# Performance work log

Measured on AMD Instinct MI355X. Metric: run time of the kernel, lower is better.

The kernel has to match this reference:

```python
import jax, jax.numpy as jnp
import numpy as np

IN_C = 128
OUT_C = 128
MEM = 512
HID = MEM // 2  # 256, per ParameterGenerator hidden_channels = memory_size // 2
T = 8          # number of edge types (keys of edge_feas_dict)
N = 500_000


def setup_inputs() -> dict:
    key = jax.random.key(0)
    ks = jax.random.split(key, 16)
    s = 0.02
    inp = {
        "x": jax.random.normal(ks[0], (N, IN_C), dtype=jnp.float32),
        "type_vec": jax.random.randint(ks[1], (N,), 0, T),
        "edge_feas": jax.random.normal(ks[2], (T, MEM), dtype=jnp.float32),
        # weight_generator MLP: Linear(MEM,HID) -> ReLU -> Linear(HID,HID) -> ReLU -> Linear(HID, IN_C*OUT_C)
        "wg_w1": jax.random.normal(ks[3], (MEM, HID), dtype=jnp.float32) * s,
        "wg_b1": jnp.zeros((HID,), dtype=jnp.float32),
        "wg_w2": jax.random.normal(ks[4], (HID, HID), dtype=jnp.float32) * s,
        "wg_b2": jnp.zeros((HID,), dtype=jnp.float32),
        "wg_w3": jax.random.normal(ks[5], (HID, IN_C * OUT_C), dtype=jnp.float32) * s,
        "wg_b3": jnp.zeros((IN_C * OUT_C,), dtype=jnp.float32),
        # bias_generator MLP: Linear(MEM,HID) -> ReLU -> Linear(HID,HID) -> ReLU -> Linear(HID, OUT_C)
        "bg_w1": jax.random.normal(ks[6], (MEM, HID), dtype=jnp.float32) * s,
        "bg_b1": jnp.zeros((HID,), dtype=jnp.float32),
        "bg_w2": jax.random.normal(ks[7], (HID, HID), dtype=jnp.float32) * s,
        "bg_b2": jnp.zeros((HID,), dtype=jnp.float32),
        "bg_w3": jax.random.normal(ks[8], (HID, OUT_C), dtype=jnp.float32) * s,
        "bg_b3": jnp.zeros((OUT_C,), dtype=jnp.float32),
    }
    return inp


def _mlp(m, w1, b1, w2, b2, w3, b3):
    h = jax.nn.relu(m @ w1 + b1)
    h = jax.nn.relu(h @ w2 + b2)
    return h @ w3 + b3


def reference(x, type_vec, edge_feas,
              wg_w1, wg_b1, wg_w2, wg_b2, wg_w3, wg_b3,
              bg_w1, bg_b1, bg_w2, bg_b2, bg_w3, bg_b3):
    # Generate per-type weights [T, IN_C, OUT_C] and biases [T, OUT_C]
    W = _mlp(edge_feas, wg_w1, wg_b1, wg_w2, wg_b2, wg_w3, wg_b3).reshape(T, IN_C, OUT_C)
    B = _mlp(edge_feas, bg_w1, bg_b1, bg_w2, bg_b2, bg_w3, bg_b3)  # [T, OUT_C]
    # Masked per-type linear, scattered back: out[n] = x[n] @ W[type_vec[n]] + B[type_vec[n]]
    out = jnp.zeros((x.shape[0], OUT_C), dtype=x.dtype)
    for t in range(T):  # small fixed set of types
        yt = x @ W[t] + B[t]
        out = jnp.where((type_vec == t)[:, None], yt, out)
    return out
```

## Files before the change

### kernel.cpp

```cpp
#include <hip/hip_runtime.h>
#include <hip/hip_bf16.h>

#define NT 8
#define MEMC 512
#define HID 256
#define C 128

typedef __attribute__((ext_vector_type(8))) short short8;
typedef __attribute__((ext_vector_type(4))) float f32x4;

__device__ inline short f2bf(float f) {
    __hip_bfloat16 h = __float2bfloat16(f);
    union { __hip_bfloat16 b; short s; } u;
    u.b = h;
    return u.s;
}

__global__ __launch_bounds__(256) void k1_init_genh(
    const float* __restrict__ edge_feas,
    const float* __restrict__ wg_w1, const float* __restrict__ wg_b1,
    const float* __restrict__ wg_w2, const float* __restrict__ wg_b2,
    const float* __restrict__ bg_w1, const float* __restrict__ bg_b1,
    const float* __restrict__ bg_w2, const float* __restrict__ bg_b2,
    int* __restrict__ hist, int* __restrict__ idx, int idx_cap,
    float* __restrict__ h_wg, float* __restrict__ h_bg,
    int n_init_blocks)
{
    int b = blockIdx.x, tid = threadIdx.x;
    if (b < n_init_blocks) {
        int pos = b * 1024 + tid * 4;
        if (pos < idx_cap) {
            int4 v = make_int4(-1, -1, -1, -1);
            *(int4*)(idx + pos) = v;
        }
        return;
    }
    if (b == n_init_blocks) {
        if (tid < NT) hist[tid] = 0;
        return;
    }
    int gb = b - n_init_blocks - 1;
    int t = gb & 7;
    int gen = gb >> 3;
    const float* w1 = gen ? bg_w1 : wg_w1;
    const float* b1 = gen ? bg_b1 : wg_b1;
    const float* w2 = gen ? bg_w2 : wg_w2;
    const float* b2 = gen ? bg_b2 : wg_b2;
    float* hout = gen ? h_bg : h_wg;

    __shared__ float m[MEMC];
    __shared__ float h1[HID];
    m[tid]       = edge_feas[t * MEMC + tid];
    m[tid + 256] = edge_feas[t * MEMC + tid + 256];
    __syncthreads();

    float a0 = b1[tid], a1 = 0.f;
    #pragma unroll 4
    for (int k = 0; k < MEMC; k += 2) {
        a0 += m[k]     * w1[k * HID + tid];
        a1 += m[k + 1] * w1[(k + 1) * HID + tid];
    }
    h1[tid] = fmaxf(a0 + a1, 0.f);
    __syncthreads();

    a0 = b2[tid]; a1 = 0.f;
    #pragma unroll 4
    for (int k = 0; k < HID; k += 2) {
        a0 += h1[k]     * w2[k * HID + tid];
        a1 += h1[k + 1] * w2[(k + 1) * HID + tid];
    }
    hout[t * HID + tid] = fmaxf(a0 + a1, 0.f);
}

__global__ __launch_bounds__(256) void k2_hist_genw(
    const int* __restrict__ type_vec, int N,
    const float* __restrict__ h_wg, const float* __restrict__ h_bg,
    const float* __restrict__ wg_w3, const float* __restrict__ wg_b3,
    const float* __restrict__ bg_w3, const float* __restrict__ bg_b3,
    int* __restrict__ hist, short* __restrict__ Wkn, float* __restrict__ Bias,
    int n_hist_blocks)
{
    int b = blockIdx.x, tid = threadIdx.x;
    if (b < n_hist_blocks) {
        __shared__ int lh[NT];
        if (tid < NT) lh[tid] = 0;
        __syncthreads();
        int base = b * 1024 + tid;
        #pragma unroll
        for (int i = 0; i < 4; ++i) {
            int n = base + i * 256;
            if (n < N) atomicAdd(&lh[type_vec[n]], 1);
        }
        __syncthreads();
        if (tid < NT) atomicAdd(&hist[tid], lh[tid]);
        return;
    }
    int gb = b - n_hist_blocks;
    if (gb < 128) {
        int chunk = gb >> 1;
        int t0 = (gb & 1) * 4;
        __shared__ float h[4][HID];
        for (int i = tid; i < 4 * HID; i += 256)
            h[i >> 8][i & 255] = h_wg[(t0 + (i >> 8)) * HID + (i & 255)];
        __syncthreads();
        int col = chunk * 256 + tid;
        float a0 = 0.f, a1 = 0.f, a2 = 0.f, a3 = 0.f;
        #pragma unroll 2
        for (int j = 0; j < HID; ++j) {
            float v = wg_w3[j * (C * C) + col];
            a0 += h[0][j] * v;
            a1 += h[1][j] * v;
            a2 += h[2][j] * v;
            a3 += h[3][j] * v;
        }
        float b3 = wg_b3[col];
        Wkn[(t0 + 0) * (C * C) + col] = f2bf(a0 + b3);
        Wkn[(t0 + 1) * (C * C) + col] = f2bf(a1 + b3);
        Wkn[(t0 + 2) * (C * C) + col] = f2bf(a2 + b3);
        Wkn[(t0 + 3) * (C * C) + col] = f2bf(a3 + b3);
        return;
    }
    if (tid < C) {
        for (int t = 0; t < NT; ++t) {
            float acc = bg_b3[tid];
            for (int j = 0; j < HID; ++j)
                acc += h_bg[t * HID + j] * bg_w3[j * C + tid];
            Bias[t * C + tid] = acc;
        }
    }
}

__global__ void k3_scan(const int* __restrict__ hist, int* __restrict__ seg,
                        int* __restrict__ cursor)
{
    if (threadIdx.x == 0) {
        int s = 0;
        for (int t = 0; t < NT; ++t) {
            seg[t] = s;
            s += ((hist[t] + 63) >> 6) << 6;
        }
        seg[NT] = s;
    }
    if (threadIdx.x < NT) cursor[threadIdx.x * 16] = 0;
}

__global__ __launch_bounds__(256) void k4_scatter_transpose(
    const int* __restrict__ type_vec, int N,
    const int* __restrict__ seg, int* __restrict__ cursor,
    int* __restrict__ idx,
    const short* __restrict__ Wkn, short* __restrict__ Wt,
    int n_scatter_blocks)
{
    int b = blockIdx.x, tid = threadIdx.x;
    if (b >= n_scatter_blocks) {
        int t = b - n_scatter_blocks;
        __shared__ short tile[C][C + 8];
        const short* src = Wkn + t * (C * C);
        for (int i = tid; i < C * C; i += 256)
            tile[i >> 7][i & 127] = src[i];
        __syncthreads();
        short* dst = Wt + t * (C * C);
        for (int i = tid; i < C * C; i += 256)
            dst[i] = tile[i & 127][i >> 7];
        return;
    }
    int lane = tid & 63;
    int wave = b * 4 + (tid >> 6);
    int start = wave * 1024;
    if (start >= N) return;

    int cnt[NT];
    #pragma unroll
    for (int t = 0; t < NT; ++t) cnt[t] = 0;
    for (int c = 0; c < 16; ++c) {
        int n = start + c * 64 + lane;
        int mt = (n < N) ? type_vec[n] : NT;
        #pragma unroll
        for (int t = 0; t < NT; ++t)
            cnt[t] += __popcll(__ballot(mt == t));
    }
    int base = 0;
    if (lane < NT) base = atomicAdd(&cursor[lane * 16], cnt[lane]);
    int run[NT];
    #pragma unroll
    for (int t = 0; t < NT; ++t) run[t] = seg[t] + __shfl(base, t, 64);
    unsigned long long below = (1ULL << lane) - 1ULL;
    for (int c = 0; c < 16; ++c) {
        int n = start + c * 64 + lane;
        int mt = (n < N) ? type_vec[n] : NT;
        int mypos = 0;
        #pragma unroll
        for (int t = 0; t < NT; ++t) {
            unsigned long long msk = __ballot(mt == t);
            if (mt == t) mypos = run[t] + __popcll(msk & below);
            run[t] += __popcll(msk);
        }
        if (n < N) idx[mypos] = n;
    }
}

__global__ __launch_bounds__(256) void k5_gemm(
    const float* __restrict__ x, const int* __restrict__ idx,
    const short* __restrict__ Wt, const float* __restrict__ Bias,
    const int* __restrict__ seg, float* __restrict__ out)
{
    int tid = threadIdx.x;
    int lane = tid & 63;
    int w = tid >> 6;
    int block_base = blockIdx.x * 64;
    int total = seg[NT];
    if (block_base >= total) return;

    int t = 0;
    #pragma unroll
    for (int i = 1; i < NT; ++i)
        if (block_base >= seg[i]) t = i;

    int quad = lane >> 4;
    int m16 = lane & 15;
    const short* Wtt = Wt + t * (C * C);

    int arow = idx[block_base + 16 * w + m16];
    bool avalid = arow >= 0;
    const float* xrow = x + (size_t)(avalid ? arow : 0) * C;

    f32x4 acc[8];
    #pragma unroll
    for (int i = 0; i < 8; ++i) acc[i] = (f32x4){0.f, 0.f, 0.f, 0.f};

    #pragma unroll
    for (int kk = 0; kk < 4; ++kk) {
        int k0 = kk * 32 + quad * 8;
        short8 afrag;
        if (avalid) {
            float4 a0 = *(const float4*)(xrow + k0);
            float4 a1 = *(const float4*)(xrow + k0 + 4);
            afrag[0] = f2bf(a0.x); afrag[1] = f2bf(a0.y);
            afrag[2] = f2bf(a0.z); afrag[3] = f2bf(a0.w);
            afrag[4] = f2bf(a1.x); afrag[5] = f2bf(a1.y);
            afrag[6] = f2bf(a1.z); afrag[7] = f2bf(a1.w);
        } else {
            afrag = (short8){0, 0, 0, 0, 0, 0, 0, 0};
        }
        #pragma unroll
        for (int ni = 0; ni < 8; ++ni) {
            short8 bfrag = *(const short8*)(Wtt + (ni * 16 + m16) * C + k0);
            acc[ni] = __builtin_amdgcn_mfma_f32_16x16x32_bf16(afrag, bfrag, acc[ni], 0, 0, 0);
        }
    }

    float bv[8];
    #pragma unroll
    for (int ni = 0; ni < 8; ++ni) bv[ni] = Bias[t * C + ni * 16 + m16];

    int p0 = block_base + 16 * w + quad * 4;
    #pragma unroll
    for (int r = 0; r < 4; ++r) {
        int node = idx[p0 + r];
        if (node < 0) continue;
        float* orow = out + (size_t)node * C;
        #pragma unroll
        for (int ni = 0; ni < 8; ++ni)
            orow[ni * 16 + m16] = acc[ni][r] + bv[ni];
    }
}

extern "C" void kernel_launch(void* const* d_in, const int* in_sizes, int n_in,
                              void* d_out, int out_size, void* d_ws, size_t ws_size,
                              hipStream_t stream)
{
    const float* x         = (const float*)d_in[0];
    const int*   type_vec  = (const int*)d_in[1];
    const float* edge_feas = (const float*)d_in[2];
    const float* wg_w1 = (const float*)d_in[3];
    const float* wg_b1 = (const float*)d_in[4];
    const float* wg_w2 = (const float*)d_in[5];
    const float* wg_b2 = (const float*)d_in[6];
    const float* wg_w3 = (const float*)d_in[7];
    const float* wg_b3 = (const float*)d_in[8];
    const float* bg_w1 = (const float*)d_in[9];
    const float* bg_b1 = (const float*)d_in[10];
    const float* bg_w2 = (const float*)d_in[11];
    const float* bg_b2 = (const float*)d_in[12];
    const float* bg_w3 = (const float*)d_in[13];
    const float* bg_b3 = (const float*)d_in[14];
    float* out = (float*)d_out;
    int N = in_sizes[1];

    char* ws = (char*)d_ws;
    int*   hist   = (int*)(ws + 0);
    int*   seg    = (int*)(ws + 64);
    int*   cursor = (int*)(ws + 128);
    float* h_wg   = (float*)(ws + 1024);
    float* h_bg   = (float*)(ws + 9216);
    float* Bias   = (float*)(ws + 17408);
    short* Wkn    = (short*)(ws + 21504);
    short* Wt     = (short*)(ws + 283648);
    int*   idx    = (int*)(ws + 545792);

    int nblk64  = (N + 63) / 64;
    int idx_cap = (nblk64 + 8) * 64;
    int n_init  = (idx_cap + 1023) / 1024;
    int n_hist  = (N + 1023) / 1024;
    int n_scat  = (n_hist + 3) / 4;

    k1_init_genh<<<n_init + 17, 256, 0, stream>>>(
        edge_feas, wg_w1, wg_b1, wg_w2, wg_b2, bg_w1, bg_b1, bg_w2, bg_b2,
        hist, idx, idx_cap, h_wg, h_bg, n_init);

    k2_hist_genw<<<n_hist + 129, 256, 0, stream>>>(
        type_vec, N, h_wg, h_bg, wg_w3, wg_b3, bg_w3, bg_b3,
        hist, Wkn, Bias, n_hist);

    k3_scan<<<1, 64, 0, stream>>>(hist, seg, cursor);

    k4_scatter_transpose<<<n_scat + 8, 256, 0, stream>>>(
        type_vec, N, seg, cursor, idx, Wkn, Wt, n_scat);

    k5_gemm<<<nblk64 + 8, 256, 0, stream>>>(x, idx, Wt, Bias, seg, out);
}
```

Baseline: 660.1 us.

## Stage gather GEMM through LDS, parallelize weight generator, drop scan kernel

New measurement: 544.9 us. 17.4% less time.

```diff
diff --git a/kernel.cpp b/kernel.cpp
--- a/kernel.cpp
+++ b/kernel.cpp
@@ -7,12 +7,12 @@
 #define C 128
 
 typedef __attribute__((ext_vector_type(8))) short short8;
+typedef __attribute__((ext_vector_type(4))) short short4v;
 typedef __attribute__((ext_vector_type(4))) float f32x4;
 
 __device__ inline short f2bf(float f) {
-    __hip_bfloat16 h = __float2bfloat16(f);
     union { __hip_bfloat16 b; short s; } u;
-    u.b = h;
+    u.b = __float2bfloat16(f);
     return u.s;
 }
 
@@ -22,21 +22,19 @@
     const float* __restrict__ wg_w2, const float* __restrict__ wg_b2,
     const float* __restrict__ bg_w1, const float* __restrict__ bg_b1,
     const float* __restrict__ bg_w2, const float* __restrict__ bg_b2,
-    int* __restrict__ hist, int* __restrict__ idx, int idx_cap,
+    int* __restrict__ hist, int* __restrict__ cursor,
+    int* __restrict__ idx, int idx_cap,
     float* __restrict__ h_wg, float* __restrict__ h_bg,
     int n_init_blocks)
 {
     int b = blockIdx.x, tid = threadIdx.x;
     if (b < n_init_blocks) {
         int pos = b * 1024 + tid * 4;
-        if (pos < idx_cap) {
-            int4 v = make_int4(-1, -1, -1, -1);
-            *(int4*)(idx + pos) = v;
-        }
+        if (pos < idx_cap) *(int4*)(idx + pos) = make_int4(-1, -1, -1, -1);
         return;
     }
     if (b == n_init_blocks) {
-        if (tid < NT) hist[tid] = 0;
+        if (tid < NT) { hist[tid] = 0; cursor[tid * 16] = 0; }
         return;
     }
     int gb = b - n_init_blocks - 1;
@@ -49,27 +47,46 @@
     float* hout = gen ? h_bg : h_wg;
 
     __shared__ float m[MEMC];
+    __shared__ float part[4][HID];
     __shared__ float h1[HID];
     m[tid]       = edge_feas[t * MEMC + tid];
     m[tid + 256] = edge_feas[t * MEMC + tid + 256];
     __syncthreads();
 
-    float a0 = b1[tid], a1 = 0.f;
-    #pragma unroll 4
-    for (int k = 0; k < MEMC; k += 2) {
-        a0 += m[k]     * w1[k * HID + tid];
-        a1 += m[k + 1] * w1[(k + 1) * HID + tid];
-    }
-    h1[tid] = fmaxf(a0 + a1, 0.f);
-    __syncthreads();
-
-    a0 = b2[tid]; a1 = 0.f;
-    #pragma unroll 4
-    for (int k = 0; k < HID; k += 2) {
-        a0 += h1[k]     * w2[k * HID + tid];
-        a1 += h1[k + 1] * w2[(k + 1) * HID + tid];
-    }
-    hout[t * HID + tid] = fmaxf(a0 + a1, 0.f);
+    int w = tid >> 6, l = tid & 63;
+    {
+        float ax = 0.f, ay = 0.f, az = 0.f, aw = 0.f;
+        const float* wp = w1 + (size_t)(w * 128) * HID + 4 * l;
+        #pragma unroll 8
+        for (int k = 0; k < 128; ++k) {
+            float4 v = *(const float4*)(wp + (size_t)k * HID);
+            float mk = m[w * 128 + k];
+            ax += mk * v.x; ay += mk * v.y; az += mk * v.z; aw += mk * v.w;
+        }
+        *(float4*)&part[w][4 * l] = make_float4(ax, ay, az, aw);
+    }
+    __syncthreads();
+    {
+        float s = part[0][tid] + part[1][tid] + part[2][tid] + part[3][tid] + b1[tid];
+        h1[tid] = fmaxf(s, 0.f);
+    }
+    __syncthreads();
+    {
+        float ax = 0.f, ay = 0.f, az = 0.f, aw = 0.f;
+        const float* wp = w2 + (size_t)(w * 64) * HID + 4 * l;
+        #pragma unroll 8
+        for (int k = 0; k < 64; ++k) {
+            float4 v = *(const float4*)(wp + (size_t)k * HID);
+            float hk = h1[w * 64 + k];
+            ax += hk * v.x; ay += hk * v.y; az += hk * v.z; aw += hk * v.w;
+        }
+        *(float4*)&part[w][4 * l] = make_float4(ax, ay, az, aw);
+    }
+    __syncthreads();
+    {
+        float s = part[0][tid] + part[1][tid] + part[2][tid] + part[3][tid] + b2[tid];
+        hout[t * HID + tid] = fmaxf(s, 0.f);
+    }
 }
 
 __global__ __launch_bounds__(256) void k2_hist_genw(
@@ -81,6 +98,8 @@
     int n_hist_blocks)
 {
     int b = blockIdx.x, tid = threadIdx.x;
+    __shared__ float sh[2048];
+    __shared__ float sp[2048];
     if (b < n_hist_blocks) {
         __shared__ int lh[NT];
         if (tid < NT) lh[tid] = 0;
@@ -96,57 +115,62 @@
         return;
     }
     int gb = b - n_hist_blocks;
-    if (gb < 128) {
-        int chunk = gb >> 1;
-        int t0 = (gb & 1) * 4;
-        __shared__ float h[4][HID];
-        for (int i = tid; i < 4 * HID; i += 256)
-            h[i >> 8][i & 255] = h_wg[(t0 + (i >> 8)) * HID + (i & 255)];
-        __syncthreads();
-        int col = chunk * 256 + tid;
-        float a0 = 0.f, a1 = 0.f, a2 = 0.f, a3 = 0.f;
-        #pragma unroll 2
-        for (int j = 0; j < HID; ++j) {
-            float v = wg_w3[j * (C * C) + col];
-            a0 += h[0][j] * v;
-            a1 += h[1][j] * v;
-            a2 += h[2][j] * v;
-            a3 += h[3][j] * v;
-        }
-        float b3 = wg_b3[col];
-        Wkn[(t0 + 0) * (C * C) + col] = f2bf(a0 + b3);
-        Wkn[(t0 + 1) * (C * C) + col] = f2bf(a1 + b3);
-        Wkn[(t0 + 2) * (C * C) + col] = f2bf(a2 + b3);
-        Wkn[(t0 + 3) * (C * C) + col] = f2bf(a3 + b3);
-        return;
-    }
-    if (tid < C) {
-        for (int t = 0; t < NT; ++t) {
-            float acc = bg_b3[tid];
-            for (int j = 0; j < HID; ++j)
-                acc += h_bg[t * HID + j] * bg_w3[j * C + tid];
-            Bias[t * C + tid] = acc;
-        }
-    }
-}
-
-__global__ void k3_scan(const int* __restrict__ hist, int* __restrict__ seg,
-                        int* __restrict__ cursor)
-{
-    if (threadIdx.x == 0) {
-        int s = 0;
-        for (int t = 0; t < NT; ++t) {
-            seg[t] = s;
-            s += ((hist[t] + 63) >> 6) << 6;
-        }
-        seg[NT] = s;
-    }
-    if (threadIdx.x < NT) cursor[threadIdx.x * 16] = 0;
+    if (gb < 256) {
+        for (int i = tid; i < 2048; i += 256) sh[i] = h_wg[i];
+        __syncthreads();
+        int cl = tid & 63, p = tid >> 6;
+        int col = gb * 64 + cl;
+        float acc[NT];
+        #pragma unroll
+        for (int t = 0; t < NT; ++t) acc[t] = 0.f;
+        const float* wp = wg_w3 + (size_t)(p * 64) * (C * C) + col;
+        #pragma unroll 8
+        for (int j = 0; j < 64; ++j) {
+            float v = wp[(size_t)j * (C * C)];
+            #pragma unroll
+            for (int t = 0; t < NT; ++t) acc[t] += sh[t * 256 + p * 64 + j] * v;
+        }
+        #pragma unroll
+        for (int t = 0; t < NT; ++t) sp[p * 512 + t * 64 + cl] = acc[t];
+        __syncthreads();
+        #pragma unroll
+        for (int r = 0; r < 2; ++r) {
+            int o = tid + 256 * r;
+            int t = o >> 6, c2 = o & 63;
+            float s = sp[t * 64 + c2] + sp[512 + t * 64 + c2]
+                    + sp[1024 + t * 64 + c2] + sp[1536 + t * 64 + c2]
+                    + wg_b3[gb * 64 + c2];
+            Wkn[t * (C * C) + gb * 64 + c2] = f2bf(s);
+        }
+        return;
+    }
+    for (int i = tid; i < 2048; i += 256) sh[i] = h_bg[i];
+    __syncthreads();
+    int cl = tid & 127, p = tid >> 7;
+    float acc[NT];
+    #pragma unroll
+    for (int t = 0; t < NT; ++t) acc[t] = 0.f;
+    const float* wp = bg_w3 + (size_t)(p * 128) * C + cl;
+    #pragma unroll 8
+    for (int j = 0; j < 128; ++j) {
+        float v = wp[(size_t)j * C];
+        #pragma unroll
+        for (int t = 0; t < NT; ++t) acc[t] += sh[t * 256 + p * 128 + j] * v;
+    }
+    #pragma unroll
+    for (int t = 0; t < NT; ++t) sp[p * 1024 + t * 128 + cl] = acc[t];
+    __syncthreads();
+    #pragma unroll
+    for (int r = 0; r < 4; ++r) {
+        int o = tid + 256 * r;
+        int t = o >> 7, c2 = o & 127;
+        Bias[t * C + c2] = sp[t * 128 + c2] + sp[1024 + t * 128 + c2] + bg_b3[c2];
+    }
 }
 
 __global__ __launch_bounds__(256) void k4_scatter_transpose(
     const int* __restrict__ type_vec, int N,
-    const int* __restrict__ seg, int* __restrict__ cursor,
+    const int* __restrict__ hist, int* __restrict__ cursor,
     int* __restrict__ idx,
     const short* __restrict__ Wkn, short* __restrict__ Wt,
     int n_scatter_blocks)
@@ -164,6 +188,12 @@
             dst[i] = tile[i & 127][i >> 7];
         return;
     }
+    int seg[NT];
+    {
+        int s = 0;
+        #pragma unroll
+        for (int t = 0; t < NT; ++t) { seg[t] = s; s += ((hist[t] + 63) >> 6) << 6; }
+    }
     int lane = tid & 63;
     int wave = b * 4 + (tid >> 6);
     int start = wave * 1024;
@@ -199,30 +229,73 @@
     }
 }
 
-__global__ __launch_bounds__(256) void k5_gemm(
+#define AS_LD 136
+#define BS_LD 136
+#define CS_LD 132
+
+__global__ __launch_bounds__(256, 3) void k5_gemm(
     const float* __restrict__ x, const int* __restrict__ idx,
     const short* __restrict__ Wt, const float* __restrict__ Bias,
-    const int* __restrict__ seg, float* __restrict__ out)
-{
+    const int* __restrict__ hist, float* __restrict__ out)
+{
+    __shared__ __align__(16) char smem[64 * AS_LD * 2 + 128 * BS_LD * 2];
+    short (*As)[AS_LD] = (short(*)[AS_LD])smem;
+    short (*Bs)[BS_LD] = (short(*)[BS_LD])(smem + 64 * AS_LD * 2);
+    float (*Cs)[CS_LD] = (float(*)[CS_LD])(smem + 64 * AS_LD * 2);
+    __shared__ int ridx[64];
+
     int tid = threadIdx.x;
-    int lane = tid & 63;
-    int w = tid >> 6;
+    int lane = tid & 63, w = tid >> 6;
     int block_base = blockIdx.x * 64;
-    int total = seg[NT];
-    if (block_base >= total) return;
-
+
+    int seg[NT + 1];
+    {
+        int s = 0;
+        #pragma unroll
+        for (int t = 0; t < NT; ++t) { seg[t] = s; s += ((hist[t] + 63) >> 6) << 6; }
+        seg[NT] = s;
+    }
+    if (block_base >= seg[NT]) return;
     int t = 0;
     #pragma unroll
     for (int i = 1; i < NT; ++i)
         if (block_base >= seg[i]) t = i;
 
-    int quad = lane >> 4;
-    int m16 = lane & 15;
-    const short* Wtt = Wt + t * (C * C);
-
-    int arow = idx[block_base + 16 * w + m16];
-    bool avalid = arow >= 0;
-    const float* xrow = x + (size_t)(avalid ? arow : 0) * C;
+    if (tid < 64) ridx[tid] = idx[block_base + tid];
+    __syncthreads();
+
+    {
+        int rbase = 16 * w + (lane >> 5);
+        int c4 = (lane & 31) * 4;
+        #pragma unroll
+        for (int i = 0; i < 8; ++i) {
+            int r = rbase + i * 2;
+            int node = ridx[r];
+            float4 v = make_float4(0.f, 0.f, 0.f, 0.f);
+            if (node >= 0) v = *(const float4*)(x + (size_t)node * C + c4);
+            short4v sv;
+            sv[0] = f2bf(v.x); sv[1] = f2bf(v.y);
+            sv[2] = f2bf(v.z); sv[3] = f2bf(v.w);
+            *(short4v*)&As[r][c4] = sv;
+        }
+    }
+    {
+        int rr = w * 32 + (lane >> 4);
+        int c8 = (lane & 15) * 8;
+        const short* src = Wt + t * (C * C);
+        #pragma unroll
+        for (int i = 0; i < 8; ++i) {
+            int r = rr + i * 4;
+            short8 v = *(const short8*)(src + r * C + c8);
+            *(short8*)&Bs[r][c8] = v;
+        }
+    }
+    __syncthreads();
+
+    int quad = lane >> 4, m16 = lane & 15;
+    float bv[8];
+    #pragma unroll
+    for (int ni = 0; ni < 8; ++ni) bv[ni] = Bias[t * C + ni * 16 + m16];
 
     f32x4 acc[8];
     #pragma unroll
@@ -230,38 +303,36 @@
 
     #pragma unroll
     for (int kk = 0; kk < 4; ++kk) {
-        int k0 = kk * 32 + quad * 8;
-        short8 afrag;
-        if (avalid) {
-            float4 a0 = *(const float4*)(xrow + k0);
-            float4 a1 = *(const float4*)(xrow + k0 + 4);
-            afrag[0] = f2bf(a0.x); afrag[1] = f2bf(a0.y);
-            afrag[2] = f2bf(a0.z); afrag[3] = f2bf(a0.w);
-            afrag[4] = f2bf(a1.x); afrag[5] = f2bf(a1.y);
-            afrag[6] = f2bf(a1.z); afrag[7] = f2bf(a1.w);
-        } else {
-            afrag = (short8){0, 0, 0, 0, 0, 0, 0, 0};
-        }
+        short8 af = *(const short8*)&As[16 * w + m16][kk * 32 + quad * 8];
         #pragma unroll
         for (int ni = 0; ni < 8; ++ni) {
-            short8 bfrag = *(const short8*)(Wtt + (ni * 16 + m16) * C + k0);
-            acc[ni] = __builtin_amdgcn_mfma_f32_16x16x32_bf16(afrag, bfrag, acc[ni], 0, 0, 0);
-        }
-    }
-
-    float bv[8];
-    #pragma unroll
-    for (int ni = 0; ni < 8; ++ni) bv[ni] = Bias[t * C + ni * 16 + m16];
-
-    int p0 = block_base + 16 * w + quad * 4;
-    #pragma unroll
-    for (int r = 0; r < 4; ++r) {
-        int node = idx[p0 + r];
-        if (node < 0) continue;
-        float* orow = out + (size_t)node * C;
-        #pragma unroll
-        for (int ni = 0; ni < 8; ++ni)
-            orow[ni * 16 + m16] = acc[ni][r] + bv[ni];
+            short8 bf = *(const short8*)&Bs[ni * 16 + m16][kk * 32 + quad * 8];
+            acc[ni] = __builtin_amdgcn_mfma_f32_16x16x32_bf16(af, bf, acc[ni], 0, 0, 0);
+        }
+    }
+    __syncthreads();
+
+    #pragma unroll
+    for (int ni = 0; ni < 8; ++ni) {
+        int colc = ni * 16 + m16;
+        #pragma unroll
+        for (int r = 0; r < 4; ++r)
+            Cs[16 * w + quad * 4 + r][colc] = acc[ni][r] + bv[ni];
+    }
+    __syncthreads();
+
+    {
+        int rbase = 16 * w + (lane >> 5);
+        int c4 = (lane & 31) * 4;
+        #pragma unroll
+        for (int i = 0; i < 8; ++i) {
+            int r = rbase + i * 2;
+            int node = ridx[r];
+            if (node >= 0) {
+                float4 v = *(const float4*)&Cs[r][c4];
+                *(float4*)(out + (size_t)node * C + c4) = v;
+            }
+        }
     }
 }
 
@@ -289,7 +360,6 @@
 
     char* ws = (char*)d_ws;
     int*   hist   = (int*)(ws + 0);
-    int*   seg    = (int*)(ws + 64);
     int*   cursor = (int*)(ws + 128);
     float* h_wg   = (float*)(ws + 1024);
     float* h_bg   = (float*)(ws + 9216);
@@ -306,16 +376,14 @@
 
     k1_init_genh<<<n_init + 17, 256, 0, stream>>>(
         edge_feas, wg_w1, wg_b1, wg_w2, wg_b2, bg_w1, bg_b1, bg_w2, bg_b2,
-        hist, idx, idx_cap, h_wg, h_bg, n_init);
-
-    k2_hist_genw<<<n_hist + 129, 256, 0, stream>>>(
+        hist, cursor, idx, idx_cap, h_wg, h_bg, n_init);
+
+    k2_hist_genw<<<n_hist + 257, 256, 0, stream>>>(
         type_vec, N, h_wg, h_bg, wg_w3, wg_b3, bg_w3, bg_b3,
         hist, Wkn, Bias, n_hist);
 
-    k3_scan<<<1, 64, 0, stream>>>(hist, seg, cursor);
-
     k4_scatter_transpose<<<n_scat + 8, 256, 0, stream>>>(
-        type_vec, N, seg, cursor, idx, Wkn, Wt, n_scat);
-
-    k5_gemm<<<nblk64 + 8, 256, 0, stream>>>(x, idx, Wt, Bias, seg, out);
-}
+        type_vec, N, hist, cursor, idx, Wkn, Wt, n_scat);
+
+    k5_gemm<<<nblk64 + 8, 256, 0, stream>>>(x, idx, Wt, Bias, hist, out);
+}
```
